# Performance work log

Measured on AMD Instinct MI355X. Metric: run time of the kernel, lower is better.

The kernel has to match this reference:

```python
import jax, jax.numpy as jnp
import numpy as np

K_LAYERS = 2   # top-k layers kept in zeta routing
K_EXPERTS = 2  # top-k experts kept in alpha routing


def _topk_sparse_softmax(logits, k):
    """Keep top-k along last axis, set rest to -inf, softmax. logits [..., N]."""
    lead = logits.shape[:-1]
    n = logits.shape[-1]
    flat = logits.reshape(-1, n)
    vals, idx = jax.lax.top_k(flat, k)                      # [R,k]
    sparse = jnp.full_like(flat, -jnp.inf)
    rows = jnp.arange(flat.shape[0])[:, None]
    sparse = sparse.at[rows, idx].set(vals)
    return jax.nn.softmax(sparse, axis=-1).reshape(*lead, n)


def _lora_layer(h, W, b, A, B, zeta_l, alpha_l):
    """One backbone Linear + gated LoRA expert mixture + ReLU.
    h [B,in], W [out,in], A [E,r,in], B [E,out,r], zeta_l [B], alpha_l [B,E].
    """
    lin = h @ W.T + b                                       # [B,out]
    t = jnp.einsum('bi,eri->ber', h, A)                     # [B,E,r]
    tw = t * alpha_l[:, :, None]                            # weight experts early
    lora_sum = jnp.einsum('ber,eor->bo', tw, B)             # [B,out]
    return jax.nn.relu(lin + zeta_l[:, None] * lora_sum)


def _routing(domain_ids, dom_emb, layer_pos, Wi1, bi1, Wi2, bi2,
             Wa1, ba1, Wa2, ba2, gate_logits, R_benefit):
    M, H = dom_emb.shape
    L = layer_pos.shape[0]
    router_inp = jnp.concatenate([
        jnp.broadcast_to(dom_emb[:, None, :], (M, L, H)),
        jnp.broadcast_to(layer_pos[None, :, :], (M, L, H)),
    ], axis=-1)                                             # [M,L,2H]
    hz = jax.nn.relu(router_inp @ Wi1.T + bi1)
    zeta_logits = (hz @ Wi2.T + bi2)[..., 0]                # [M,L]
    zeta_all = _topk_sparse_softmax(zeta_logits, K_LAYERS)
    ha = jax.nn.relu(router_inp @ Wa1.T + ba1)
    alpha_logits = ha @ Wa2.T + ba2                         # [M,L,E]
    alpha_all = _topk_sparse_softmax(alpha_logits, K_EXPERTS)
    # gated benefit matrix, row-normalized
    R = jax.nn.softplus(gate_logits) * R_benefit
    R = R / jnp.clip(R.sum(-1, keepdims=True), 1e-12)
    zeta_agg = R @ zeta_all                                 # [M,L]
    alpha_agg = jnp.einsum('mn,nle->mle', R, alpha_all)     # [M,L,E]
    return zeta_agg[domain_ids], alpha_agg[domain_ids]      # [B,L],[B,L,E]


def setup_inputs() -> dict:
    key = jax.random.key(0)
    ks = jax.random.split(key, 32)
    Bsz, D0, D1, D2, D3 = 16384, 2048, 2048, 1024, 512
    E, r, M, H, L = 4, 8, 8, 64, 3
    s = 0.02
    return {
        'x': jax.random.normal(ks[0], (Bsz, D0), jnp.float32),
        'domain_ids': jax.random.randint(ks[1], (Bsz,), 0, M),
        'W1': jax.random.normal(ks[2], (D1, D0)) * s, 'b1': jnp.zeros((D1,)),
        'W2': jax.random.normal(ks[3], (D2, D1)) * s, 'b2': jnp.zeros((D2,)),
        'W3': jax.random.normal(ks[4], (D3, D2)) * s, 'b3': jnp.zeros((D3,)),
        'A1': jax.random.normal(ks[5], (E, r, D0)) * s, 'B1': jax.random.normal(ks[6], (E, D1, r)) * s,
        'A2': jax.random.normal(ks[7], (E, r, D1)) * s, 'B2': jax.random.normal(ks[8], (E, D2, r)) * s,
        'A3': jax.random.normal(ks[9], (E, r, D2)) * s, 'B3': jax.random.normal(ks[10], (E, D3, r)) * s,
        'dom_emb': jax.random.normal(ks[11], (M, H)) * s,
        'layer_pos': jax.random.normal(ks[12], (L, H)) * s,
        'Wi1': jax.random.normal(ks[13], (H, 2 * H)) * 0.1, 'bi1': jnp.zeros((H,)),
        'Wi2': jax.random.normal(ks[14], (1, H)) * 0.1, 'bi2': jnp.zeros((1,)),
        'Wa1': jax.random.normal(ks[15], (H, 2 * H)) * 0.1, 'ba1': jnp.zeros((H,)),
        'Wa2': jax.random.normal(ks[16], (E, H)) * 0.1, 'ba2': jnp.zeros((E,)),
        'gate_logits': jax.random.normal(ks[17], (M, M)) * 0.1,
        'R_benefit': jax.random.uniform(ks[18], (M, M)),
    }


def reference(x, domain_ids, W1, b1, W2, b2, W3, b3,
              A1, B1, A2, B2, A3, B3,
              dom_emb, layer_pos, Wi1, bi1, Wi2, bi2,
              Wa1, ba1, Wa2, ba2, gate_logits, R_benefit):
    zeta, alpha = _routing(domain_ids, dom_emb, layer_pos, Wi1, bi1, Wi2, bi2,
                           Wa1, ba1, Wa2, ba2, gate_logits, R_benefit)
    h = _lora_layer(x, W1, b1, A1, B1, zeta[:, 0], alpha[:, 0])
    h = _lora_layer(h, W2, b2, A2, B2, zeta[:, 1], alpha[:, 1])
    h = _lora_layer(h, W3, b3, A3, B3, zeta[:, 2], alpha[:, 2])
    return h
```

## Files before the change

kernel.cpp:

```cpp
#include <hip/hip_runtime.h>

typedef __bf16 bf16_t;
typedef __bf16 bf16x8 __attribute__((ext_vector_type(8)));
typedef __bf16 bf16x4_v __attribute__((ext_vector_type(4)));
typedef float f32x4 __attribute__((ext_vector_type(4)));

#define AS1 __attribute__((address_space(1)))
#define AS3 __attribute__((address_space(3)))

__device__ __forceinline__ void gload_lds16(const void* g, void* l) {
    __builtin_amdgcn_global_load_lds((AS1 void*)(void*)g, (AS3 void*)l, 16, 0, 0);
}

__global__ void __launch_bounds__(256) prep_kernel(
    const float* __restrict__ dom_emb, const float* __restrict__ layer_pos,
    const float* __restrict__ Wi1, const float* __restrict__ bi1,
    const float* __restrict__ Wi2, const float* __restrict__ bi2,
    const float* __restrict__ Wa1, const float* __restrict__ ba1,
    const float* __restrict__ Wa2, const float* __restrict__ ba2,
    const float* __restrict__ gate_logits, const float* __restrict__ R_benefit,
    float* __restrict__ salpha,
    const float* __restrict__ s0, const float* __restrict__ s1,
    const float* __restrict__ s2, const float* __restrict__ s3,
    const float* __restrict__ s4, const float* __restrict__ s5,
    bf16_t* __restrict__ wdst,
    const float* __restrict__ B1, const float* __restrict__ B2,
    const float* __restrict__ B3, bf16_t* __restrict__ bedst,
    const float* __restrict__ x, bf16_t* __restrict__ xb)
{
    const int blk = blockIdx.x;
    const int t = threadIdx.x;
    if (blk == 0) {
        constexpr int M = 8, L = 3, E = 4, H = 64;
        __shared__ float zl[M * L];
        __shared__ float al[M * L][E];
        __shared__ float zeta_all[M][L];
        __shared__ float alpha_all[M][L][E];
        const int ml = t >> 3, js = t & 7;
        if (ml < M * L) {
            const int m = ml / L, l = ml % L;
            float zacc = 0.f;
            float aacc[E] = {0.f, 0.f, 0.f, 0.f};
            for (int jj = 0; jj < 8; ++jj) {
                const int j = js * 8 + jj;
                float hz = bi1[j], ha = ba1[j];
                for (int i = 0; i < H; ++i) {
                    const float de = dom_emb[m * H + i];
                    const float lp = layer_pos[l * H + i];
                    hz += de * Wi1[j * 2 * H + i] + lp * Wi1[j * 2 * H + H + i];
                    ha += de * Wa1[j * 2 * H + i] + lp * Wa1[j * 2 * H + H + i];
                }
                hz = fmaxf(hz, 0.f); ha = fmaxf(ha, 0.f);
                zacc += hz * Wi2[j];
                for (int e = 0; e < E; ++e) aacc[e] += ha * Wa2[e * H + j];
            }
            #pragma unroll
            for (int off = 4; off >= 1; off >>= 1) {
                zacc += __shfl_down(zacc, off, 8);
                for (int e = 0; e < E; ++e) aacc[e] += __shfl_down(aacc[e], off, 8);
            }
            if (js == 0) {
                zl[ml] = zacc + bi2[0];
                for (int e = 0; e < E; ++e) al[ml][e] = aacc[e] + ba2[e];
            }
        }
        __syncthreads();
        if (t < M) {
            const int m = t;
            float v[3] = { zl[m * L + 0], zl[m * L + 1], zl[m * L + 2] };
            int di = 0; float dv = v[0];
            for (int i = 1; i < 3; ++i) if (v[i] <= dv) { dv = v[i]; di = i; }
            float mx = -1e30f;
            for (int i = 0; i < 3; ++i) if (i != di) mx = fmaxf(mx, v[i]);
            float s = 0.f, ev[3];
            for (int i = 0; i < 3; ++i) { ev[i] = (i == di) ? 0.f : expf(v[i] - mx); s += ev[i]; }
            for (int i = 0; i < 3; ++i) zeta_all[m][i] = ev[i] / s;
            for (int l = 0; l < L; ++l) {
                float a[4];
                for (int e = 0; e < 4; ++e) a[e] = al[m * L + l][e];
                int i1 = 0;
                for (int e = 1; e < 4; ++e) if (a[e] > a[i1]) i1 = e;
                int i2 = -1;
                for (int e = 0; e < 4; ++e) { if (e == i1) continue; if (i2 < 0 || a[e] > a[i2]) i2 = e; }
                const float mx2 = fmaxf(a[i1], a[i2]);
                const float e1 = expf(a[i1] - mx2), e2 = expf(a[i2] - mx2);
                const float ss = e1 + e2;
                for (int e = 0; e < 4; ++e) alpha_all[m][l][e] = 0.f;
                alpha_all[m][l][i1] = e1 / ss;
                alpha_all[m][l][i2] = e2 / ss;
            }
        }
        __syncthreads();
        if (t < M) {
            const int m = t;
            float Rrow[8]; float rs = 0.f;
            for (int n = 0; n < M; ++n) {
                const float g = gate_logits[m * M + n];
                const float rr = log1pf(expf(g)) * R_benefit[m * M + n];
                Rrow[n] = rr; rs += rr;
            }
            rs = fmaxf(rs, 1e-12f);
            for (int l = 0; l < L; ++l) {
                float zag = 0.f, aag[4] = {0.f, 0.f, 0.f, 0.f};
                for (int n = 0; n < M; ++n) {
                    const float w = Rrow[n] / rs;
                    zag += w * zeta_all[n][l];
                    for (int e = 0; e < 4; ++e) aag[e] += w * alpha_all[n][l][e];
                }
                for (int e = 0; e < 4; ++e) salpha[(m * L + l) * 4 + e] = zag * aag[e];
            }
        }
    } else if (blk <= 6816) {
        const int i = (blk - 1) * 256 + t;
        constexpr int b0 = 1048576;
        constexpr int b1 = b0 + 524288;
        constexpr int b2 = b1 + 131072;
        constexpr int b3 = b2 + 16384;
        constexpr int b4 = b3 + 16384;
        const float* src; int rel;
        if (i < b0)      { src = s0; rel = i; }
        else if (i < b1) { src = s1; rel = i - b0; }
        else if (i < b2) { src = s2; rel = i - b1; }
        else if (i < b3) { src = s3; rel = i - b2; }
        else if (i < b4) { src = s4; rel = i - b3; }
        else             { src = s5; rel = i - b4; }
        const float4 v = ((const float4*)src)[rel];
        bf16x4_v o;
        o[0] = (__bf16)v.x; o[1] = (__bf16)v.y; o[2] = (__bf16)v.z; o[3] = (__bf16)v.w;
        ((bf16x4_v*)wdst)[i] = o;
    } else if (blk <= 7264) {
        const int idx = (blk - 6817) * 256 + t;
        constexpr int c1 = 2048 * 32, c2 = c1 + 1024 * 32;
        const float* B; int rel, Dout;
        if (idx < c1)      { B = B1; rel = idx;      Dout = 2048; }
        else if (idx < c2) { B = B2; rel = idx - c1; Dout = 1024; }
        else               { B = B3; rel = idx - c2; Dout = 512; }
        const int o = rel >> 5, c = rel & 31, e = c >> 3, r = c & 7;
        bedst[idx] = (__bf16)B[((size_t)e * Dout + o) * 8 + r];
    } else {
        const size_t i8 = ((size_t)(blk - 7265) * 256 + t) * 8;
        const float4 v0 = *(const float4*)(x + i8);
        const float4 v1 = *(const float4*)(x + i8 + 4);
        bf16x8 o;
        o[0] = (__bf16)v0.x; o[1] = (__bf16)v0.y; o[2] = (__bf16)v0.z; o[3] = (__bf16)v0.w;
        o[4] = (__bf16)v1.x; o[5] = (__bf16)v1.y; o[6] = (__bf16)v1.z; o[7] = (__bf16)v1.w;
        *(bf16x8*)(xb + i8) = o;
    }
}

__global__ void __launch_bounds__(512) tw_kernel(
    const bf16_t* __restrict__ hin,
    const bf16_t* __restrict__ Acat, const float* __restrict__ salpha,
    const int* __restrict__ dom, const int layer, const int K,
    bf16_t* __restrict__ TWb)
{
    __shared__ float red[4 * 64 * 8];
    const int t = threadIdx.x, wid = t >> 6, lane = t & 63;
    const int g = wid & 3, h = wid >> 2;
    const int rb = blockIdx.x * 64 + g * 16;
    const int ln15 = lane & 15, kg = (lane >> 4) * 8;
    const int row = rb + ln15;
    const int Kh = K >> 1, Kq = K >> 2;
    const int base = h * Kh;
    f32x4 a0l = {0.f,0.f,0.f,0.f}, a1l = {0.f,0.f,0.f,0.f};
    f32x4 a0h = {0.f,0.f,0.f,0.f}, a1h = {0.f,0.f,0.f,0.f};
    const bf16_t* ph  = hin + (size_t)row * K + base + kg;
    const bf16_t* pa0 = Acat + (size_t)ln15 * K + base + kg;
    const bf16_t* pa1 = pa0 + (size_t)16 * K;
    for (int k0 = 0; k0 < Kq; k0 += 32) {
        const bf16x8 al  = *(const bf16x8*)(ph + k0);
        const bf16x8 ah  = *(const bf16x8*)(ph + Kq + k0);
        const bf16x8 b0l = *(const bf16x8*)(pa0 + k0);
        const bf16x8 b1l = *(const bf16x8*)(pa1 + k0);
        const bf16x8 b0h = *(const bf16x8*)(pa0 + Kq + k0);
        const bf16x8 b1h = *(const bf16x8*)(pa1 + Kq + k0);
        a0l = __builtin_amdgcn_mfma_f32_16x16x32_bf16(al, b0l, a0l, 0, 0, 0);
        a1l = __builtin_amdgcn_mfma_f32_16x16x32_bf16(al, b1l, a1l, 0, 0, 0);
        a0h = __builtin_amdgcn_mfma_f32_16x16x32_bf16(ah, b0h, a0h, 0, 0, 0);
        a1h = __builtin_amdgcn_mfma_f32_16x16x32_bf16(ah, b1h, a1h, 0, 0, 0);
    }
    f32x4 acc0 = a0l + a0h;
    f32x4 acc1 = a1l + a1h;
    float* slot = red + ((g * 64 + lane) << 3);
    if (h == 1) {
        *(f32x4*)slot = acc0;
        *(f32x4*)(slot + 4) = acc1;
    }
    __syncthreads();
    if (h == 0) {
        acc0 += *(const f32x4*)slot;
        acc1 += *(const f32x4*)(slot + 4);
        const int rbase = rb + (lane >> 4) * 4;
        #pragma unroll
        for (int i = 0; i < 4; ++i) {
            const int r2 = rbase + i;
            const int d = dom[r2];
            const float* sa = salpha + (d * 3 + layer) * 4;
            const float s0 = sa[ln15 >> 3];
            const float s1 = sa[2 + (ln15 >> 3)];
            TWb[(size_t)r2 * 32 + ln15]      = (__bf16)(acc0[i] * s0);
            TWb[(size_t)r2 * 32 + 16 + ln15] = (__bf16)(acc1[i] * s1);
        }
    }
}


__device__ __forceinline__ void stage_chunk32(const bf16_t* g, char* chunk, int t) {
    const int row = t >> 2;
    const int sl = t & 3;
    const int src = sl ^ (((row >> 3) & 1) << 1);
    gload_lds16(g + (size_t)row * 32 + src * 8, chunk + t * 16);
}

template<int K>
__global__ void __launch_bounds__(512, 2) gemm_lora8(
    const bf16_t* __restrict__ Abuf, const bf16_t* __restrict__ Wbuf,
    const float* __restrict__ bias, const bf16_t* __restrict__ TWb,
    const bf16_t* __restrict__ Bepi, bf16_t* __restrict__ outp,
    const int N, const int nwg_n)
{
    __shared__ __align__(1024) char lds[131072];
    const int t = threadIdx.x;
    const int wid = t >> 6, lane = t & 63;
    const int wm = wid >> 2, wn = wid & 3, wnh = wn >> 1;
    const int cpx = gridDim.x >> 3;
    const int wg = (blockIdx.x & 7) * cpx + (blockIdx.x >> 3);
    const int row0 = (wg / nwg_n) * 256, col0 = (wg % nwg_n) * 256;

    const int r15 = lane & 15;
    const int swb = ((lane >> 4) ^ (((lane >> 3) & 1) << 1)) << 4;

    const char* aBase = lds + (wm << 14) + (r15 << 6) + swb;
    const char* bBase = lds + 65536 + (wnh << 14) + ((wn & 1) << 12) + (r15 << 6) + swb;
    char* const dBase = lds + t * 16;

    const int srow = t >> 2, ssl = t & 3;
    const int ssrc = ssl ^ (((srow >> 3) & 1) << 1);
    const bf16_t* sA = Abuf + (size_t)(row0 + srow) * K + ssrc * 8;
    const bf16_t* sB = Wbuf + (size_t)(col0 + srow) * K + ssrc * 8;
    constexpr size_t halfA = (size_t)128 * K;

    f32x4 acc[8][4] = {};
    bf16x8 aF[4], bF[4];

    #define RD_A(P, KQ, MB) do { _Pragma("unroll") for (int i_ = 0; i_ < 4; ++i_) \
        aF[i_] = *(const bf16x8*)(aBase + (P)*32768 + (KQ)*8192 + ((MB)+i_)*1024); } while (0)
    #define RD_B(P, KQ) do { _Pragma("unroll") for (int n_ = 0; n_ < 4; ++n_) \
        bF[n_] = *(const bf16x8*)(bBase + (P)*32768 + (KQ)*8192 + n_*1024); } while (0)

    auto mfma16 = [&](int mbase) {
        __builtin_amdgcn_s_setprio(1);
        #pragma unroll
        for (int mf = 0; mf < 4; ++mf)
            #pragma unroll
            for (int nf = 0; nf < 4; ++nf)
                acc[mbase + mf][nf] =
                    __builtin_amdgcn_mfma_f32_16x16x32_bf16(aF[mf], bF[nf], acc[mbase + mf][nf], 0, 0, 0);
        __builtin_amdgcn_s_setprio(0);
    };
    #define BAR() __builtin_amdgcn_s_barrier()

    constexpr int NT = K >> 6;

    gload_lds16(sA,              dBase + 0);
    gload_lds16(sA + halfA,      dBase + 16384);
    gload_lds16(sB,              dBase + 65536);
    gload_lds16(sB + halfA,      dBase + 65536 + 16384);
    gload_lds16(sA + 32,         dBase + 8192);
    gload_lds16(sA + halfA + 32, dBase + 24576);
    gload_lds16(sB + 32,         dBase + 65536 + 8192);
    gload_lds16(sB + halfA + 32, dBase + 65536 + 24576);
    asm volatile("s_waitcnt vmcnt(4)" ::: "memory");
    __builtin_amdgcn_s_barrier();

    const bf16_t* pA0 = sA + 64;
    const bf16_t* pA1 = sA + halfA + 64;
    const bf16_t* pB0 = sB + 64;
    const bf16_t* pB1 = sB + halfA + 64;

    #define TILE(P, MORE, TOFF) do {                                            \
        RD_A(P, 0, 0);                                                           \
        RD_B(P, 0);                                                              \
        if (MORE) { gload_lds16(pA0 + (TOFF), dBase + ((P)^1)*32768 + 0);        \
                    gload_lds16(pA1 + (TOFF), dBase + ((P)^1)*32768 + 16384); }  \
        BAR();                                                                   \
        mfma16(0);                                                               \
        RD_A(P, 0, 4);                                                           \
        if (MORE) {                                                              \
            gload_lds16(pB0 + (TOFF), dBase + 65536 + ((P)^1)*32768 + 0);        \
            gload_lds16(pB1 + (TOFF), dBase + 65536 + ((P)^1)*32768 + 16384);    \
            asm volatile("s_waitcnt vmcnt(4)" ::: "memory");                     \
        } else {                                                                 \
            asm volatile("s_waitcnt vmcnt(0)" ::: "memory");                     \
        }                                                                        \
        BAR();                                                                   \
        mfma16(4);                                                               \
        RD_A(P, 1, 4);                                                           \
        RD_B(P, 1);                                                              \
        if (MORE) { gload_lds16(pA0 + (TOFF) + 32, dBase + ((P)^1)*32768 + 8192);  \
                    gload_lds16(pA1 + (TOFF) + 32, dBase + ((P)^1)*32768 + 24576);} \
        BAR();                                                                   \
        mfma16(4);                                                               \
        RD_A(P, 1, 0);                                                           \
        if (MORE) {                                                              \
            gload_lds16(pB0 + (TOFF) + 32, dBase + 65536 + ((P)^1)*32768 + 8192);  \
            gload_lds16(pB1 + (TOFF) + 32, dBase + 65536 + ((P)^1)*32768 + 24576); \
            asm volatile("s_waitcnt vmcnt(4)" ::: "memory");                     \
        }                                                                        \
        BAR();                                                                   \
        mfma16(0);                                                               \
    } while (0)

    #pragma unroll 1
    for (int T = 0; T < NT - 2; T += 2) {
        TILE(0, true, 0);
        TILE(1, true, 64);
        pA0 += 128; pA1 += 128; pB0 += 128; pB1 += 128;
    }
    TILE(0, true, 0);
    TILE(1, false, 64);

    {
        __builtin_amdgcn_s_barrier();
        stage_chunk32(TWb + (size_t)row0 * 32,          lds + 0,             t);
        stage_chunk32(TWb + (size_t)(row0 + 128) * 32,  lds + 16384,         t);
        stage_chunk32(Bepi + (size_t)col0 * 32,         lds + 65536,         t);
        stage_chunk32(Bepi + (size_t)(col0 + 128) * 32, lds + 65536 + 16384, t);
        asm volatile("s_waitcnt vmcnt(0)" ::: "memory");
        __builtin_amdgcn_s_barrier();
        RD_B(0, 0);
        RD_A(0, 0, 0);
        mfma16(0);
        RD_A(0, 0, 4);
        mfma16(4);
    }

    __builtin_amdgcn_s_barrier();
    {
        char* eb = lds + wid * 2048;
        const int rloc = (lane >> 4) * 4;
        const int g = lane >> 4;
        const int orow0 = row0 + wm * 128;
        const int ocol0 = col0 + wn * 64;
        float bcol[4];
        #pragma unroll
        for (int nf = 0; nf < 4; ++nf) bcol[nf] = bias[ocol0 + nf * 16 + r15];
        const int rdrow = lane >> 3;
        const int rdcolb = (lane & 7) * 16;
        const int rdoff0 = rdrow * 128 + (rdcolb ^ ((rdrow >> 2) << 5));
        const int rdoff1 = (rdrow + 8) * 128 + (rdcolb ^ (((rdrow + 8) >> 2) << 5));
        bf16_t* outbase = outp + (size_t)ocol0 + (lane & 7) * 8;
        #pragma unroll
        for (int mf = 0; mf < 8; ++mf) {
            #pragma unroll
            for (int i = 0; i < 4; ++i) {
                const int r = rloc + i;
                #pragma unroll
                for (int nf = 0; nf < 4; ++nf) {
                    const float v = fmaxf(acc[mf][nf][i] + bcol[nf], 0.f);
                    *(bf16_t*)(eb + r * 128 + ((nf ^ g) * 32 + r15 * 2)) = (__bf16)v;
                }
            }
            __builtin_amdgcn_sched_barrier(0);
            asm volatile("" ::: "memory");
            const bf16x8 v0 = *(const bf16x8*)(eb + rdoff0);
            const bf16x8 v1 = *(const bf16x8*)(eb + rdoff1);
            asm volatile("" ::: "memory");
            __builtin_amdgcn_sched_barrier(0);
            *(bf16x8*)(outbase + (size_t)(orow0 + mf * 16 + rdrow) * N) = v0;
            *(bf16x8*)(outbase + (size_t)(orow0 + mf * 16 + 8 + rdrow) * N) = v1;
        }
    }
    #undef TILE
    #undef RD_A
    #undef RD_B
    #undef BAR
}

#define BM 128
#define BN 128
#define BK 32

template<bool OUT_F32, int K>
__global__ void __launch_bounds__(256) gemm_lora(
    const bf16_t* __restrict__ Abuf, const bf16_t* __restrict__ Wbuf,
    const float* __restrict__ bias, const bf16_t* __restrict__ TWb,
    const bf16_t* __restrict__ Bepi, void* __restrict__ outp,
    const int N)
{
    __shared__ bf16_t lA[BM * BK];
    __shared__ bf16_t lB[BN * BK];
    const int t = threadIdx.x;
    const int row0 = blockIdx.y * BM;
    const int col0 = blockIdx.x * BN;
    const int wid = t >> 6, lane = t & 63;
    const int wr = wid >> 1, wc = wid & 1;
    const int ln15 = lane & 15, kg = (lane >> 4) * 8;
    const int srow = t >> 2, sg8 = (t & 3) * 8;
    const bf16_t* gA = Abuf + (size_t)(row0 + srow) * K + sg8;
    const bf16_t* gB = Wbuf + (size_t)(col0 + srow) * K + sg8;
    bf16_t* ldA  = &lA[t * 8];
    bf16_t* ldA2 = &lA[2048 + t * 8];
    bf16_t* ldB  = &lB[t * 8];
    bf16_t* ldB2 = &lB[2048 + t * 8];
    f32x4 acc[4][4] = {};
    const int aoff = (wr * 64 + ln15) * BK + kg;
    const int boff = (wc * 64 + ln15) * BK + kg;

    auto compute_tile = [&]() {
        bf16x8 af[4], bfr[4];
        #pragma unroll
        for (int m = 0; m < 4; ++m) af[m] = *(const bf16x8*)&lA[aoff + m * 16 * BK];
        #pragma unroll
        for (int n = 0; n < 4; ++n) bfr[n] = *(const bf16x8*)&lB[boff + n * 16 * BK];
        #pragma unroll
        for (int m = 0; m < 4; ++m)
            #pragma unroll
            for (int n = 0; n < 4; ++n)
                acc[m][n] = __builtin_amdgcn_mfma_f32_16x16x32_bf16(af[m], bfr[n], acc[m][n], 0, 0, 0);
    };

    constexpr size_t half = (size_t)64 * K;
    constexpr int nk = K / BK;
    #pragma unroll 1
    for (int kt = 0; kt < nk; ++kt) {
        gload_lds16(gA + kt * BK, ldA);
        gload_lds16(gA + half + kt * BK, ldA2);
        gload_lds16(gB + kt * BK, ldB);
        gload_lds16(gB + half + kt * BK, ldB2);
        __syncthreads();
        compute_tile();
        __syncthreads();
    }
    gload_lds16(TWb + (size_t)(row0 + srow) * 32 + sg8, ldA);
    gload_lds16(TWb + (size_t)(row0 + 64 + srow) * 32 + sg8, ldA2);
    gload_lds16(Bepi + (size_t)(col0 + srow) * 32 + sg8, ldB);
    gload_lds16(Bepi + (size_t)(col0 + 64 + srow) * 32 + sg8, ldB2);
    __syncthreads();
    compute_tile();

    const int orow = row0 + wr * 64 + (lane >> 4) * 4;
    const int ocol = col0 + wc * 64 + ln15;
    #pragma unroll
    for (int n = 0; n < 4; ++n) {
        const int col = ocol + n * 16;
        const float bn = bias[col];
        #pragma unroll
        for (int m = 0; m < 4; ++m) {
            const int rbase = orow + m * 16;
            #pragma unroll
            for (int i = 0; i < 4; ++i) {
                const float v = fmaxf(acc[m][n][i] + bn, 0.f);
                if constexpr (OUT_F32)
                    ((float*)outp)[(size_t)(rbase + i) * N + col] = v;
                else
                    ((bf16_t*)outp)[(size_t)(rbase + i) * N + col] = (__bf16)v;
            }
        }
    }
}

extern "C" void kernel_launch(void* const* d_in, const int* in_sizes, int n_in,
                              void* d_out, int out_size, void* d_ws, size_t ws_size,
                              hipStream_t stream)
{
    const float* x    = (const float*)d_in[0];
    const int*   dom  = (const int*)d_in[1];
    const float* W1   = (const float*)d_in[2];  const float* b1  = (const float*)d_in[3];
    const float* W2   = (const float*)d_in[4];  const float* b2  = (const float*)d_in[5];
    const float* W3   = (const float*)d_in[6];  const float* b3  = (const float*)d_in[7];
    const float* A1   = (const float*)d_in[8];  const float* B1  = (const float*)d_in[9];
    const float* A2   = (const float*)d_in[10]; const float* B2  = (const float*)d_in[11];
    const float* A3   = (const float*)d_in[12]; const float* B3  = (const float*)d_in[13];
    const float* dome = (const float*)d_in[14]; const float* lpos = (const float*)d_in[15];
    const float* Wi1  = (const float*)d_in[16]; const float* bi1 = (const float*)d_in[17];
    const float* Wi2  = (const float*)d_in[18]; const float* bi2 = (const float*)d_in[19];
    const float* Wa1  = (const float*)d_in[20]; const float* ba1 = (const float*)d_in[21];
    const float* Wa2  = (const float*)d_in[22]; const float* ba2 = (const float*)d_in[23];
    const float* gate = (const float*)d_in[24]; const float* Rb  = (const float*)d_in[25];
    (void)in_sizes; (void)n_in; (void)out_size; (void)ws_size;

    constexpr int Bsz = 16384, D0 = 2048, D1 = 2048, D2 = 1024, D3 = 512;

    char* ws = (char*)d_ws;
    size_t off = 0;
    auto alloc = [&](size_t bytes) -> void* {
        void* p = ws + off;
        off = (off + bytes + 255) & ~(size_t)255;
        return p;
    };
    float*  salpha = (float*) alloc(8 * 3 * 4 * sizeof(float));
    bf16_t* W1b = (bf16_t*)alloc((size_t)D1 * D0 * 2);
    bf16_t* W2b = (bf16_t*)alloc((size_t)D2 * D1 * 2);
    bf16_t* W3b = (bf16_t*)alloc((size_t)D3 * D2 * 2);
    bf16_t* Ac1 = (bf16_t*)alloc((size_t)32 * D0 * 2);
    bf16_t* Ac2 = (bf16_t*)alloc((size_t)32 * D1 * 2);
    bf16_t* Ac3 = (bf16_t*)alloc((size_t)32 * D2 * 2);
    bf16_t* Be1 = (bf16_t*)alloc((size_t)D1 * 32 * 2);
    bf16_t* Be2 = (bf16_t*)alloc((size_t)D2 * 32 * 2);
    bf16_t* Be3 = (bf16_t*)alloc((size_t)D3 * 32 * 2);
    bf16_t* TWb = (bf16_t*)alloc((size_t)Bsz * 32 * 2);
    bf16_t* xb  = (bf16_t*)alloc((size_t)Bsz * D0 * 2);
    bf16_t* h1b = (bf16_t*)alloc((size_t)Bsz * D1 * 2);
    bf16_t* h2b = xb;

    prep_kernel<<<23649, 256, 0, stream>>>(
        dome, lpos, Wi1, bi1, Wi2, bi2, Wa1, ba1, Wa2, ba2, gate, Rb, salpha,
        W1, W2, W3, A1, A2, A3, W1b,
        B1, B2, B3, Be1,
        x, xb);

    tw_kernel<<<Bsz / 64, 512, 0, stream>>>(xb, Ac1, salpha, dom, 0, D0, TWb);
    gemm_lora8<2048><<<(Bsz / 256) * (D1 / 256), 512, 0, stream>>>(xb, W1b, b1, TWb, Be1, h1b, D1, D1 / 256);
    tw_kernel<<<Bsz / 64, 512, 0, stream>>>(h1b, Ac2, salpha, dom, 1, D1, TWb);
    gemm_lora8<2048><<<(Bsz / 256) * (D2 / 256), 512, 0, stream>>>(h1b, W2b, b2, TWb, Be2, h2b, D2, D2 / 256);
    tw_kernel<<<Bsz / 64, 512, 0, stream>>>(h2b, Ac3, salpha, dom, 2, D2, TWb);
    gemm_lora<true, 1024><<<dim3(D3 / BN, Bsz / BM), 256, 0, stream>>>(h2b, W3b, b3, TWb, Be3, d_out, D3);
}
```

Baseline: 358.8 us.

## Fuse LoRA down-projection into main GEMM mainloop, drop separate tw_kernel

Removes the three standalone tw_kernel launches that computed h@A^T scaled by alpha. Each GEMM now also stages the 32-row Acat slice into extra LDS and runs extra MFMAs on the A fragments it already loaded, then scales by alpha in the epilogue and writes the result into LDS for the LoRA up-projection. This saves three kernel launches and a second full read of the activations. In exchange it adds LDS use (143 KB in gemm_lora8, which may limit occupancy under launch_bounds(512,2)), extra MFMAs, and recomputes the down-projection redundantly in every column-tile workgroup.

```diff
diff --git a/kernel.cpp b/kernel.cpp
--- a/kernel.cpp
+++ b/kernel.cpp
@@ -148,62 +148,9 @@
     }
 }
 
-__global__ void __launch_bounds__(512) tw_kernel(
-    const bf16_t* __restrict__ hin,
-    const bf16_t* __restrict__ Acat, const float* __restrict__ salpha,
-    const int* __restrict__ dom, const int layer, const int K,
-    bf16_t* __restrict__ TWb)
-{
-    __shared__ float red[4 * 64 * 8];
-    const int t = threadIdx.x, wid = t >> 6, lane = t & 63;
-    const int g = wid & 3, h = wid >> 2;
-    const int rb = blockIdx.x * 64 + g * 16;
-    const int ln15 = lane & 15, kg = (lane >> 4) * 8;
-    const int row = rb + ln15;
-    const int Kh = K >> 1, Kq = K >> 2;
-    const int base = h * Kh;
-    f32x4 a0l = {0.f,0.f,0.f,0.f}, a1l = {0.f,0.f,0.f,0.f};
-    f32x4 a0h = {0.f,0.f,0.f,0.f}, a1h = {0.f,0.f,0.f,0.f};
-    const bf16_t* ph  = hin + (size_t)row * K + base + kg;
-    const bf16_t* pa0 = Acat + (size_t)ln15 * K + base + kg;
-    const bf16_t* pa1 = pa0 + (size_t)16 * K;
-    for (int k0 = 0; k0 < Kq; k0 += 32) {
-        const bf16x8 al  = *(const bf16x8*)(ph + k0);
-        const bf16x8 ah  = *(const bf16x8*)(ph + Kq + k0);
-        const bf16x8 b0l = *(const bf16x8*)(pa0 + k0);
-        const bf16x8 b1l = *(const bf16x8*)(pa1 + k0);
-        const bf16x8 b0h = *(const bf16x8*)(pa0 + Kq + k0);
-        const bf16x8 b1h = *(const bf16x8*)(pa1 + Kq + k0);
-        a0l = __builtin_amdgcn_mfma_f32_16x16x32_bf16(al, b0l, a0l, 0, 0, 0);
-        a1l = __builtin_amdgcn_mfma_f32_16x16x32_bf16(al, b1l, a1l, 0, 0, 0);
-        a0h = __builtin_amdgcn_mfma_f32_16x16x32_bf16(ah, b0h, a0h, 0, 0, 0);
-        a1h = __builtin_amdgcn_mfma_f32_16x16x32_bf16(ah, b1h, a1h, 0, 0, 0);
-    }
-    f32x4 acc0 = a0l + a0h;
-    f32x4 acc1 = a1l + a1h;
-    float* slot = red + ((g * 64 + lane) << 3);
-    if (h == 1) {
-        *(f32x4*)slot = acc0;
-        *(f32x4*)(slot + 4) = acc1;
-    }
-    __syncthreads();
-    if (h == 0) {
-        acc0 += *(const f32x4*)slot;
-        acc1 += *(const f32x4*)(slot + 4);
-        const int rbase = rb + (lane >> 4) * 4;
-        #pragma unroll
-        for (int i = 0; i < 4; ++i) {
-            const int r2 = rbase + i;
-            const int d = dom[r2];
-            const float* sa = salpha + (d * 3 + layer) * 4;
-            const float s0 = sa[ln15 >> 3];
-            const float s1 = sa[2 + (ln15 >> 3)];
-            TWb[(size_t)r2 * 32 + ln15]      = (__bf16)(acc0[i] * s0);
-            TWb[(size_t)r2 * 32 + 16 + ln15] = (__bf16)(acc1[i] * s1);
-        }
-    }
-}
-
+
+#define ACBASE  131072
+#define ACDUMMY 139264
 
 __device__ __forceinline__ void stage_chunk32(const bf16_t* g, char* chunk, int t) {
     const int row = t >> 2;
@@ -215,11 +162,12 @@
 template<int K>
 __global__ void __launch_bounds__(512, 2) gemm_lora8(
     const bf16_t* __restrict__ Abuf, const bf16_t* __restrict__ Wbuf,
-    const float* __restrict__ bias, const bf16_t* __restrict__ TWb,
+    const float* __restrict__ bias, const bf16_t* __restrict__ Acat,
     const bf16_t* __restrict__ Bepi, bf16_t* __restrict__ outp,
-    const int N, const int nwg_n)
+    const int N, const int nwg_n,
+    const int* __restrict__ domv, const float* __restrict__ salpha, const int layer)
 {
-    __shared__ __align__(1024) char lds[131072];
+    __shared__ __align__(1024) char lds[143360];
     const int t = threadIdx.x;
     const int wid = t >> 6, lane = t & 63;
     const int wm = wid >> 2, wn = wid & 3, wnh = wn >> 1;
@@ -234,19 +182,35 @@
     const char* bBase = lds + 65536 + (wnh << 14) + ((wn & 1) << 12) + (r15 << 6) + swb;
     char* const dBase = lds + t * 16;
 
+    const char* acBase2 = lds + ACBASE + (r15 << 7);
+    const int acsw0 = (((lane >> 4)) ^ (r15 & 7)) << 4;
+    const int acsw1 = ((4 + (lane >> 4)) ^ (r15 & 7)) << 4;
+
     const int srow = t >> 2, ssl = t & 3;
     const int ssrc = ssl ^ (((srow >> 3) & 1) << 1);
     const bf16_t* sA = Abuf + (size_t)(row0 + srow) * K + ssrc * 8;
     const bf16_t* sB = Wbuf + (size_t)(col0 + srow) * K + ssrc * 8;
     constexpr size_t halfA = (size_t)128 * K;
 
+    const int tt = t & 255;
+    const int acrow = tt >> 3;
+    const bf16_t* sAc = Acat + (size_t)acrow * K + (((tt & 7) ^ (acrow & 7)) * 8);
+    char* const acD0 = (t < 256) ? (lds + ACBASE + tt * 16)        : (lds + ACDUMMY + tt * 16);
+    char* const acD1 = (t < 256) ? (lds + ACBASE + 4096 + tt * 16) : (lds + ACDUMMY + tt * 16);
+
     f32x4 acc[8][4] = {};
-    bf16x8 aF[4], bF[4];
+    f32x4 twacc[2][2] = {};
+    bf16x8 aF[4], bF[4], acF[2];
 
     #define RD_A(P, KQ, MB) do { _Pragma("unroll") for (int i_ = 0; i_ < 4; ++i_) \
         aF[i_] = *(const bf16x8*)(aBase + (P)*32768 + (KQ)*8192 + ((MB)+i_)*1024); } while (0)
     #define RD_B(P, KQ) do { _Pragma("unroll") for (int n_ = 0; n_ < 4; ++n_) \
         bF[n_] = *(const bf16x8*)(bBase + (P)*32768 + (KQ)*8192 + n_*1024); } while (0)
+    #define RD_AC(P, KQ) do { _Pragma("unroll") for (int n_ = 0; n_ < 2; ++n_) \
+        acF[n_] = *(const bf16x8*)(acBase2 + (P)*4096 + n_*2048 + ((KQ) ? acsw1 : acsw0)); } while (0)
+    #define TW_MM() do { _Pragma("unroll") for (int mp_ = 0; mp_ < 2; ++mp_) \
+        _Pragma("unroll") for (int n_ = 0; n_ < 2; ++n_) \
+        twacc[mp_][n_] = __builtin_amdgcn_mfma_f32_16x16x32_bf16(aF[2*(wn&1)+mp_], acF[n_], twacc[mp_][n_], 0, 0, 0); } while (0)
 
     auto mfma16 = [&](int mbase) {
         __builtin_amdgcn_s_setprio(1);
@@ -264,6 +228,7 @@
 
     gload_lds16(sA,              dBase + 0);
     gload_lds16(sA + halfA,      dBase + 16384);
+    gload_lds16(sAc,             acD0);
     gload_lds16(sB,              dBase + 65536);
     gload_lds16(sB + halfA,      dBase + 65536 + 16384);
     gload_lds16(sA + 32,         dBase + 8192);
@@ -277,31 +242,40 @@
     const bf16_t* pA1 = sA + halfA + 64;
     const bf16_t* pB0 = sB + 64;
     const bf16_t* pB1 = sB + halfA + 64;
+    const bf16_t* pAc = sAc + 64;
 
     #define TILE(P, MORE, TOFF) do {                                            \
         RD_A(P, 0, 0);                                                           \
         RD_B(P, 0);                                                              \
+        if (wn < 2) RD_AC(P, 0);                                                 \
         if (MORE) { gload_lds16(pA0 + (TOFF), dBase + ((P)^1)*32768 + 0);        \
-                    gload_lds16(pA1 + (TOFF), dBase + ((P)^1)*32768 + 16384); }  \
+                    gload_lds16(pA1 + (TOFF), dBase + ((P)^1)*32768 + 16384);    \
+                    gload_lds16(pAc + (TOFF), (P) ? acD0 : acD1); }              \
         BAR();                                                                   \
         mfma16(0);                                                               \
+        if (wn < 2) TW_MM();                                                     \
         RD_A(P, 0, 4);                                                           \
+        if (wn >= 2) RD_AC(P, 0);                                                \
         if (MORE) {                                                              \
             gload_lds16(pB0 + (TOFF), dBase + 65536 + ((P)^1)*32768 + 0);        \
             gload_lds16(pB1 + (TOFF), dBase + 65536 + ((P)^1)*32768 + 16384);    \
-            asm volatile("s_waitcnt vmcnt(4)" ::: "memory");                     \
+            asm volatile("s_waitcnt vmcnt(5)" ::: "memory");                     \
         } else {                                                                 \
             asm volatile("s_waitcnt vmcnt(0)" ::: "memory");                     \
         }                                                                        \
         BAR();                                                                   \
         mfma16(4);                                                               \
+        if (wn >= 2) TW_MM();                                                    \
         RD_A(P, 1, 4);                                                           \
         RD_B(P, 1);                                                              \
+        if (wn >= 2) RD_AC(P, 1);                                                \
         if (MORE) { gload_lds16(pA0 + (TOFF) + 32, dBase + ((P)^1)*32768 + 8192);  \
                     gload_lds16(pA1 + (TOFF) + 32, dBase + ((P)^1)*32768 + 24576);} \
         BAR();                                                                   \
         mfma16(4);                                                               \
+        if (wn >= 2) TW_MM();                                                    \
         RD_A(P, 1, 0);                                                           \
+        if (wn < 2) RD_AC(P, 1);                                                 \
         if (MORE) {                                                              \
             gload_lds16(pB0 + (TOFF) + 32, dBase + 65536 + ((P)^1)*32768 + 8192);  \
             gload_lds16(pB1 + (TOFF) + 32, dBase + 65536 + ((P)^1)*32768 + 24576); \
@@ -309,24 +283,44 @@
         }                                                                        \
         BAR();                                                                   \
         mfma16(0);                                                               \
+        if (wn < 2) TW_MM();                                                     \
     } while (0)
 
     #pragma unroll 1
     for (int T = 0; T < NT - 2; T += 2) {
         TILE(0, true, 0);
         TILE(1, true, 64);
-        pA0 += 128; pA1 += 128; pB0 += 128; pB1 += 128;
+        pA0 += 128; pA1 += 128; pB0 += 128; pB1 += 128; pAc += 128;
     }
     TILE(0, true, 0);
     TILE(1, false, 64);
 
     {
+        asm volatile("" ::: "memory");
         __builtin_amdgcn_s_barrier();
-        stage_chunk32(TWb + (size_t)row0 * 32,          lds + 0,             t);
-        stage_chunk32(TWb + (size_t)(row0 + 128) * 32,  lds + 16384,         t);
         stage_chunk32(Bepi + (size_t)col0 * 32,         lds + 65536,         t);
         stage_chunk32(Bepi + (size_t)(col0 + 128) * 32, lds + 65536 + 16384, t);
-        asm volatile("s_waitcnt vmcnt(0)" ::: "memory");
+        const int i16 = lane >> 4;
+        #pragma unroll
+        for (int mp_ = 0; mp_ < 2; ++mp_) {
+            const int mfg = 2 * wn + mp_;
+            #pragma unroll
+            for (int i_ = 0; i_ < 4; ++i_) {
+                const int rl = mfg * 16 + i16 * 4 + i_;
+                const int d = domv[row0 + wm * 128 + rl];
+                const float* sa = salpha + (d * 3 + layer) * 4;
+                #pragma unroll
+                for (int n_ = 0; n_ < 2; ++n_) {
+                    const int c = n_ * 16 + r15;
+                    const float s = sa[n_ * 2 + (r15 >> 3)];
+                    const float v = twacc[mp_][n_][i_] * s;
+                    *(bf16_t*)(lds + (wm << 14) + rl * 64 +
+                               (((c >> 3) ^ (((rl >> 3) & 1) << 1)) << 4) + ((c & 7) << 1)) = (__bf16)v;
+                }
+            }
+        }
+        asm volatile("s_waitcnt vmcnt(0) lgkmcnt(0)" ::: "memory");
+        __builtin_amdgcn_sched_barrier(0);
         __builtin_amdgcn_s_barrier();
         RD_B(0, 0);
         RD_A(0, 0, 0);
@@ -374,6 +368,8 @@
     #undef TILE
     #undef RD_A
     #undef RD_B
+    #undef RD_AC
+    #undef TW_MM
     #undef BAR
 }
 
@@ -384,12 +380,14 @@
 template<bool OUT_F32, int K>
 __global__ void __launch_bounds__(256) gemm_lora(
     const bf16_t* __restrict__ Abuf, const bf16_t* __restrict__ Wbuf,
-    const float* __restrict__ bias, const bf16_t* __restrict__ TWb,
+    const float* __restrict__ bias, const bf16_t* __restrict__ Acat,
     const bf16_t* __restrict__ Bepi, void* __restrict__ outp,
-    const int N)
+    const int N,
+    const int* __restrict__ domv, const float* __restrict__ salpha)
 {
     __shared__ bf16_t lA[BM * BK];
     __shared__ bf16_t lB[BN * BK];
+    __shared__ bf16_t lAc[32 * BK];
     const int t = threadIdx.x;
     const int row0 = blockIdx.y * BM;
     const int col0 = blockIdx.x * BN;
@@ -404,11 +402,12 @@
     bf16_t* ldB  = &lB[t * 8];
     bf16_t* ldB2 = &lB[2048 + t * 8];
     f32x4 acc[4][4] = {};
+    f32x4 twacc[4] = {};
+    bf16x8 af[4], bfr[4];
     const int aoff = (wr * 64 + ln15) * BK + kg;
     const int boff = (wc * 64 + ln15) * BK + kg;
 
     auto compute_tile = [&]() {
-        bf16x8 af[4], bfr[4];
         #pragma unroll
         for (int m = 0; m < 4; ++m) af[m] = *(const bf16x8*)&lA[aoff + m * 16 * BK];
         #pragma unroll
@@ -428,12 +427,32 @@
         gload_lds16(gA + half + kt * BK, ldA2);
         gload_lds16(gB + kt * BK, ldB);
         gload_lds16(gB + half + kt * BK, ldB2);
+        if (t < 128)
+            gload_lds16(Acat + (size_t)(t >> 2) * K + kt * BK + (t & 3) * 8, (char*)lAc + t * 16);
         __syncthreads();
         compute_tile();
+        {
+            const bf16x8 acatF = *(const bf16x8*)&lAc[(wc * 16 + ln15) * BK + kg];
+            #pragma unroll
+            for (int m = 0; m < 4; ++m)
+                twacc[m] = __builtin_amdgcn_mfma_f32_16x16x32_bf16(af[m], acatF, twacc[m], 0, 0, 0);
+        }
         __syncthreads();
     }
-    gload_lds16(TWb + (size_t)(row0 + srow) * 32 + sg8, ldA);
-    gload_lds16(TWb + (size_t)(row0 + 64 + srow) * 32 + sg8, ldA2);
+    {
+        const int i16 = lane >> 4;
+        #pragma unroll
+        for (int m = 0; m < 4; ++m) {
+            #pragma unroll
+            for (int i = 0; i < 4; ++i) {
+                const int r = wr * 64 + m * 16 + i16 * 4 + i;
+                const int d = domv[row0 + r];
+                const int c = wc * 16 + ln15;
+                const float s = salpha[(d * 3 + 2) * 4 + wc * 2 + (ln15 >> 3)];
+                lA[r * BK + c] = (__bf16)(twacc[m][i] * s);
+            }
+        }
+    }
     gload_lds16(Bepi + (size_t)(col0 + srow) * 32 + sg8, ldB);
     gload_lds16(Bepi + (size_t)(col0 + 64 + srow) * 32 + sg8, ldB2);
     __syncthreads();
@@ -499,7 +518,6 @@
     bf16_t* Be1 = (bf16_t*)alloc((size_t)D1 * 32 * 2);
     bf16_t* Be2 = (bf16_t*)alloc((size_t)D2 * 32 * 2);
     bf16_t* Be3 = (bf16_t*)alloc((size_t)D3 * 32 * 2);
-    bf16_t* TWb = (bf16_t*)alloc((size_t)Bsz * 32 * 2);
     bf16_t* xb  = (bf16_t*)alloc((size_t)Bsz * D0 * 2);
     bf16_t* h1b = (bf16_t*)alloc((size_t)Bsz * D1 * 2);
     bf16_t* h2b = xb;
@@ -510,10 +528,10 @@
         B1, B2, B3, Be1,
         x, xb);
 
-    tw_kernel<<<Bsz / 64, 512, 0, stream>>>(xb, Ac1, salpha, dom, 0, D0, TWb);
-    gemm_lora8<2048><<<(Bsz / 256) * (D1 / 256), 512, 0, stream>>>(xb, W1b, b1, TWb, Be1, h1b, D1, D1 / 256);
-    tw_kernel<<<Bsz / 64, 512, 0, stream>>>(h1b, Ac2, salpha, dom, 1, D1, TWb);
-    gemm_lora8<2048><<<(Bsz / 256) * (D2 / 256), 512, 0, stream>>>(h1b, W2b, b2, TWb, Be2, h2b, D2, D2 / 256);
-    tw_kernel<<<Bsz / 64, 512, 0, stream>>>(h2b, Ac3, salpha, dom, 2, D2, TWb);
-    gemm_lora<true, 1024><<<dim3(D3 / BN, Bsz / BM), 256, 0, stream>>>(h2b, W3b, b3, TWb, Be3, d_out, D3);
+    gemm_lora8<2048><<<(Bsz / 256) * (D1 / 256), 512, 0, stream>>>(
+        xb, W1b, b1, Ac1, Be1, h1b, D1, D1 / 256, dom, salpha, 0);
+    gemm_lora8<2048><<<(Bsz / 256) * (D2 / 256), 512, 0, stream>>>(
+        h1b, W2b, b2, Ac2, Be2, h2b, D2, D2 / 256, dom, salpha, 1);
+    gemm_lora<true, 1024><<<dim3(D3 / BN, Bsz / BM), 256, 0, stream>>>(
+        h2b, W3b, b3, Ac3, Be3, d_out, D3, dom, salpha);
 }
```

Result: slower. 678.3 us (+89.0%).

## Fuse layer-3 LoRA down-projection into final GEMM, dropping tw_kernel launch

Applied to the files above, without the earlier changes.

The third layer's tw_kernel launch is removed. Each block of the final GEMM now loads a 32-row slice of the concatenated LoRA A matrix alongside the main tiles and accumulates the down-projection with extra MFMAs that reuse the already-loaded A fragments. The result is scaled by the per-domain alpha/zeta factor and written to shared memory for the epilogue. This saves a kernel launch and a global round-trip of the TW buffer, but every output-column block recomputes the same down-projection, which adds redundant MFMA work and extra LDS traffic.

```diff
diff --git a/kernel.cpp b/kernel.cpp
--- a/kernel.cpp
+++ b/kernel.cpp
@@ -384,12 +384,14 @@
 template<bool OUT_F32, int K>
 __global__ void __launch_bounds__(256) gemm_lora(
     const bf16_t* __restrict__ Abuf, const bf16_t* __restrict__ Wbuf,
-    const float* __restrict__ bias, const bf16_t* __restrict__ TWb,
+    const float* __restrict__ bias, const bf16_t* __restrict__ Acat,
     const bf16_t* __restrict__ Bepi, void* __restrict__ outp,
-    const int N)
+    const int N,
+    const int* __restrict__ domv, const float* __restrict__ salpha)
 {
     __shared__ bf16_t lA[BM * BK];
     __shared__ bf16_t lB[BN * BK];
+    __shared__ bf16_t lAc[32 * BK];
     const int t = threadIdx.x;
     const int row0 = blockIdx.y * BM;
     const int col0 = blockIdx.x * BN;
@@ -404,11 +406,12 @@
     bf16_t* ldB  = &lB[t * 8];
     bf16_t* ldB2 = &lB[2048 + t * 8];
     f32x4 acc[4][4] = {};
+    f32x4 twacc[4] = {};
+    bf16x8 af[4], bfr[4];
     const int aoff = (wr * 64 + ln15) * BK + kg;
     const int boff = (wc * 64 + ln15) * BK + kg;
 
     auto compute_tile = [&]() {
-        bf16x8 af[4], bfr[4];
         #pragma unroll
         for (int m = 0; m < 4; ++m) af[m] = *(const bf16x8*)&lA[aoff + m * 16 * BK];
         #pragma unroll
@@ -428,12 +431,32 @@
         gload_lds16(gA + half + kt * BK, ldA2);
         gload_lds16(gB + kt * BK, ldB);
         gload_lds16(gB + half + kt * BK, ldB2);
+        if (t < 128)
+            gload_lds16(Acat + (size_t)(t >> 2) * K + kt * BK + (t & 3) * 8, (char*)lAc + t * 16);
         __syncthreads();
         compute_tile();
+        {
+            const bf16x8 acatF = *(const bf16x8*)&lAc[(wc * 16 + ln15) * BK + kg];
+            #pragma unroll
+            for (int m = 0; m < 4; ++m)
+                twacc[m] = __builtin_amdgcn_mfma_f32_16x16x32_bf16(af[m], acatF, twacc[m], 0, 0, 0);
+        }
         __syncthreads();
     }
-    gload_lds16(TWb + (size_t)(row0 + srow) * 32 + sg8, ldA);
-    gload_lds16(TWb + (size_t)(row0 + 64 + srow) * 32 + sg8, ldA2);
+    {
+        const int i16 = lane >> 4;
+        #pragma unroll
+        for (int m = 0; m < 4; ++m) {
+            #pragma unroll
+            for (int i = 0; i < 4; ++i) {
+                const int r = wr * 64 + m * 16 + i16 * 4 + i;
+                const int d = domv[row0 + r];
+                const int c = wc * 16 + ln15;
+                const float s = salpha[(d * 3 + 2) * 4 + wc * 2 + (ln15 >> 3)];
+                lA[r * BK + c] = (__bf16)(twacc[m][i] * s);
+            }
+        }
+    }
     gload_lds16(Bepi + (size_t)(col0 + srow) * 32 + sg8, ldB);
     gload_lds16(Bepi + (size_t)(col0 + 64 + srow) * 32 + sg8, ldB2);
     __syncthreads();
@@ -514,6 +537,6 @@
     gemm_lora8<2048><<<(Bsz / 256) * (D1 / 256), 512, 0, stream>>>(xb, W1b, b1, TWb, Be1, h1b, D1, D1 / 256);
     tw_kernel<<<Bsz / 64, 512, 0, stream>>>(h1b, Ac2, salpha, dom, 1, D1, TWb);
     gemm_lora8<2048><<<(Bsz / 256) * (D2 / 256), 512, 0, stream>>>(h1b, W2b, b2, TWb, Be2, h2b, D2, D2 / 256);
-    tw_kernel<<<Bsz / 64, 512, 0, stream>>>(h2b, Ac3, salpha, dom, 2, D2, TWb);
-    gemm_lora<true, 1024><<<dim3(D3 / BN, Bsz / BM), 256, 0, stream>>>(h2b, W3b, b3, TWb, Be3, d_out, D3);
-}
+    gemm_lora<true, 1024><<<dim3(D3 / BN, Bsz / BM), 256, 0, stream>>>(
+        h2b, W3b, b3, Ac3, Be3, d_out, D3, dom, salpha);
+}
```

New measurement: 346.3 us. -3.5%, faster.
